# Kernel tuning notes

Hardware: AMD Instinct MI355X
Metric: run time of the kernel (lower is better)

## Reference

```python
import jax, jax.numpy as jnp
import numpy as np

D = 512
H = 8
FFN_H = 2048
NEG = -1.0e10


def layer_norm(x, gamma, beta, eps=1e-5):
    mu = jnp.mean(x, axis=-1, keepdims=True)
    var = jnp.var(x, axis=-1, keepdims=True)
    return (x - mu) * jax.lax.rsqrt(var + eps) * gamma + beta


def mha(x_q, x_kv, Wq, Wk, Wv, Wo, valid_lens):
    # x_q: [B,Tq,D], x_kv: [B,Tk,D]; valid_lens: [B,Tq] or [B]
    B, Tq, _ = x_q.shape
    Tk = x_kv.shape[1]
    dh = D // H
    q = (x_q @ Wq.T).reshape(B, Tq, H, dh).transpose(0, 2, 1, 3)  # [B,H,Tq,dh]
    k = (x_kv @ Wk.T).reshape(B, Tk, H, dh).transpose(0, 2, 1, 3)
    v = (x_kv @ Wv.T).reshape(B, Tk, H, dh).transpose(0, 2, 1, 3)
    scores = jnp.einsum('bhqd,bhkd->bhqk', q, k) / jnp.sqrt(jnp.float32(dh))
    pos = jnp.arange(Tk)
    if valid_lens.ndim == 1:  # [B] -> mask [B,1,1,Tk]
        mask = pos[None, None, None, :] < valid_lens[:, None, None, None]
    else:  # [B,Tq] -> mask [B,1,Tq,Tk]
        mask = pos[None, None, None, :] < valid_lens[:, None, :, None]
    scores = jnp.where(mask, scores, NEG)
    attn = jax.nn.softmax(scores, axis=-1)
    out = jnp.einsum('bhqk,bhkd->bhqd', attn, v)  # [B,H,Tq,dh]
    out = out.transpose(0, 2, 1, 3).reshape(B, Tq, D)
    return out @ Wo.T


def setup_inputs() -> dict:
    key = jax.random.key(0)
    ks = jax.random.split(key, 20)
    B, T = 32, 512
    s = 1.0 / np.sqrt(D)
    inp = {
        'X': jax.random.normal(ks[0], (B, T, D), jnp.float32),
        'enc_outputs': jax.random.normal(ks[1], (B, T, D), jnp.float32),
        'dec_valid_lens': jax.random.randint(ks[2], (B, T), 1, T + 1, jnp.int32),
        'enc_valid_lens': jax.random.randint(ks[3], (B,), 1, T + 1, jnp.int32),
    }
    names = ['Wq1', 'Wk1', 'Wv1', 'Wo1', 'Wq2', 'Wk2', 'Wv2', 'Wo2']
    for i, n in enumerate(names):
        inp[n] = jax.random.normal(ks[4 + i], (D, D), jnp.float32) * s
    inp['W1'] = jax.random.normal(ks[12], (FFN_H, D), jnp.float32) * s
    inp['b1'] = jnp.zeros((FFN_H,), jnp.float32)
    inp['W2'] = jax.random.normal(ks[13], (D, FFN_H), jnp.float32) * (1.0 / np.sqrt(FFN_H))
    inp['b2'] = jnp.zeros((D,), jnp.float32)
    for j in (1, 2, 3):
        inp[f'g{j}'] = jnp.ones((D,), jnp.float32)
        inp[f'be{j}'] = jnp.zeros((D,), jnp.float32)
    return inp


def reference(X, enc_outputs, dec_valid_lens, enc_valid_lens,
              Wq1, Wk1, Wv1, Wo1, Wq2, Wk2, Wv2, Wo2,
              W1, b1, W2, b2, g1, be1, g2, be2, g3, be3):
    # Training path: state[2][i] is None -> key_values = X. Dropout in eval mode (identity).
    X2 = mha(X, X, Wq1, Wk1, Wv1, Wo1, dec_valid_lens)            # self-attention
    Y = layer_norm(X + X2, g1, be1)                               # AddNorm1
    Y2 = mha(Y, enc_outputs, Wq2, Wk2, Wv2, Wo2, enc_valid_lens)  # cross-attention
    Z = layer_norm(Y + Y2, g2, be2)                               # AddNorm2
    F = (jax.nn.leaky_relu(Z @ W1.T + b1, 0.01)) @ W2.T + b2      # FFN (LeakyReLU slope 0.01)
    return layer_norm(Z + F, g3, be3)                             # AddNorm3
```

## Files before the change

### kernel.cpp

```cpp
#include <hip/hip_runtime.h>
#include <cstdint>
#include <cstddef>

typedef __bf16 bf16;
typedef __bf16 bf16x8 __attribute__((ext_vector_type(8)));
typedef float  f32x4  __attribute__((ext_vector_type(4)));
typedef unsigned short u16;

#define MD ((size_t)8388608)

__device__ __forceinline__ void async_copy16(const bf16* gp, bf16* lp) {
  __builtin_amdgcn_global_load_lds(
      (__attribute__((address_space(1))) void*)(gp),
      (__attribute__((address_space(3))) void*)(lp), 16, 0, 0);
}

__device__ __forceinline__ int is_f32(const u16* __restrict__ x) {
  const int e = (x[(threadIdx.x & 63) * 2] >> 7) & 0xFF;
  return __ballot(e >= 141) != 0ull;
}

struct ConvSrc { const void* p[20]; };

__global__ __launch_bounds__(256)
void convert_all(ConvSrc s, bf16* __restrict__ ws, const u16* __restrict__ xprobe)
{
  const int n[20] = {8388608, 8388608,
                     262144, 262144, 262144, 262144, 262144, 262144, 262144, 262144,
                     1048576, 2048, 1048576, 512, 512, 512, 512, 512, 512, 512};
  const unsigned int doff[20] = {
      41943040u, 50331648u,
      58720256u, 58982400u, 59244544u, 59506688u,
      59768832u, 60030976u, 60293120u, 60555264u,
      60817408u, 61865984u, 61868032u, 62916608u,
      62917120u, 62917632u, 62918144u, 62918656u, 62919168u, 62919680u};

  const int f32 = is_f32(xprobe);

  int bi = blockIdx.x;
  int idx = 0, b0 = 0;
  for (; idx < 20; ++idx) {
    const int nb = (n[idx] + 2047) >> 11;
    if (bi < b0 + nb) break;
    b0 += nb;
  }
  const int i = ((bi - b0) << 11) + threadIdx.x * 8;
  if (i >= n[idx]) return;
  bf16* dst = ws + doff[idx] + i;
  if (f32) {
    const float* sp = (const float*)s.p[idx] + i;
    f32x4 a = *(const f32x4*)sp;
    f32x4 b = *(const f32x4*)(sp + 4);
    bf16x8 o;
#pragma unroll
    for (int e = 0; e < 4; ++e) { o[e] = (bf16)a[e]; o[4 + e] = (bf16)b[e]; }
    *(bf16x8*)dst = o;
  } else {
    *(bf16x8*)dst = *(const bf16x8*)((const bf16*)s.p[idx] + i);
  }
}

template<int MODE, int TM, int TN>
__global__ __launch_bounds__(256)
void gemm_bt(const bf16* __restrict__ A, const bf16* __restrict__ B,
             const bf16* __restrict__ bias, bf16* __restrict__ C,
             int M, int N, int K)
{
  constexpr int MI = TM / 32;
  constexpr int NJ = TN / 32;
  __shared__ __attribute__((aligned(16))) bf16 As[TM * 64];
  __shared__ __attribute__((aligned(16))) bf16 Bs[TN * 64];

  const int t    = threadIdx.x;
  const int wave = t >> 6;
  const int lane = t & 63;
  const int quad = lane >> 4;
  const int l15  = lane & 15;
  const int wr   = (wave >> 1) * (TM / 2);
  const int wc   = (wave & 1) * (TN / 2);

  const int id    = blockIdx.y * gridDim.x + blockIdx.x;
  const int chunk = (gridDim.x * gridDim.y) >> 3;
  const int lin   = (id & 7) * chunk + (id >> 3);
  const int m0    = (lin / gridDim.x) * TM;
  const int n0    = (lin % gridDim.x) * TN;

  const f32x4 fz = {0.f, 0.f, 0.f, 0.f};
  f32x4 acc[MI][NJ];
#pragma unroll
  for (int i = 0; i < MI; ++i)
#pragma unroll
    for (int j = 0; j < NJ; ++j) acc[i][j] = fz;

  const int nkt = K >> 6;
  for (int kt = 0; kt < nkt; ++kt) {
    const int k0 = kt << 6;
    __syncthreads();
#pragma unroll
    for (int c = 0; c < TM / 32; ++c) {
      const int s   = c * 256 + t;
      const int row = s >> 3;
      const int kg  = ((s & 7) ^ (row & 7)) << 3;
      async_copy16(A + (size_t)(m0 + row) * K + k0 + kg,
                   As + ((c * 256 + wave * 64) << 3));
    }
#pragma unroll
    for (int c = 0; c < TN / 32; ++c) {
      const int s   = c * 256 + t;
      const int row = s >> 3;
      const int kg  = ((s & 7) ^ (row & 7)) << 3;
      async_copy16(B + (size_t)(n0 + row) * K + k0 + kg,
                   Bs + ((c * 256 + wave * 64) << 3));
    }
    __syncthreads();

#pragma unroll
    for (int ks = 0; ks < 2; ++ks) {
      bf16x8 af[MI], bfv[NJ];
#pragma unroll
      for (int i = 0; i < MI; ++i) {
        const int row = wr + i * 16 + l15;
        const int ph  = (ks * 4 + quad) ^ (row & 7);
        af[i] = *(const bf16x8*)(As + row * 64 + ph * 8);
      }
#pragma unroll
      for (int j = 0; j < NJ; ++j) {
        const int row = wc + j * 16 + l15;
        const int ph  = (ks * 4 + quad) ^ (row & 7);
        bfv[j] = *(const bf16x8*)(Bs + row * 64 + ph * 8);
      }
#pragma unroll
      for (int i = 0; i < MI; ++i)
#pragma unroll
        for (int j = 0; j < NJ; ++j)
          acc[i][j] = __builtin_amdgcn_mfma_f32_16x16x32_bf16(af[i], bfv[j],
                                                              acc[i][j], 0, 0, 0);
    }
  }

#pragma unroll
  for (int i = 0; i < MI; ++i) {
    const int m = m0 + wr + i * 16 + quad * 4;
#pragma unroll
    for (int j = 0; j < NJ; ++j) {
      const int n = n0 + wc + j * 16 + l15;
      float bv = 0.f;
      if (MODE >= 1) bv = (float)bias[n];
#pragma unroll
      for (int r = 0; r < 4; ++r) {
        float v = acc[i][j][r];
        if (MODE >= 1) v += bv;
        if (MODE == 1) v = v > 0.f ? v : 0.01f * v;
        C[(size_t)(m + r) * N + n] = (bf16)v;
      }
    }
  }
}

template<int MODE>
__global__ __launch_bounds__(512, 1)
void gemm4p(const bf16* __restrict__ A, const bf16* __restrict__ B,
            const bf16* __restrict__ bias, bf16* __restrict__ C,
            int M, int N, int K)
{
  constexpr int BM = 256, BN = 256, WM = 2, WN = 4, T = 512;
  constexpr int WR = BM / WM;
  constexpr int MI = WR / 16;
  constexpr int NJ = (BN / WN) / 16;
  constexpr int MH = MI / 2;
  constexpr int LA = BM * 8 / T;
  constexpr int LB = BN * 8 / T;
  static_assert(LA == 4 && LB == 4 && NJ == 4, "schedule assumes 4/4/4");

  __shared__ __attribute__((aligned(16))) bf16 As[2][BM * 64];
  __shared__ __attribute__((aligned(16))) bf16 Bs[2][BN * 64];

  const int t    = threadIdx.x;
  const int lane = t & 63;
  const int quad = lane >> 4;
  const int l15  = lane & 15;
  const int wave = t >> 6;
  const int wm   = wave >> 2;
  const int wn   = wave & 3;

  const int id    = blockIdx.y * gridDim.x + blockIdx.x;
  const int chunk = (gridDim.x * gridDim.y) >> 3;
  const int lin   = (id & 7) * chunk + (id >> 3);
  const int m0    = (lin / gridDim.x) * BM;
  const int n0    = (lin % gridDim.x) * BN;

  const bf16* Ag = A + (size_t)m0 * K;
  const bf16* Bg = B + (size_t)n0 * K;
  const int wbase = wave << 6;

  auto stA = [&](int kt, int r, int buf) {
    const int s   = r * T + t;
    const int row = s >> 3;
    const int cg  = s & 7;
    async_copy16(Ag + (size_t)row * K + (kt << 6) + ((cg ^ (row & 7)) << 3),
                 &As[buf][(size_t)(r * T + wbase) << 3]);
  };
  auto stB = [&](int kt, int r, int buf) {
    const int s   = r * T + t;
    const int row = s >> 3;
    const int cg  = s & 7;
    async_copy16(Bg + (size_t)row * K + (kt << 6) + ((cg ^ (row & 7)) << 3),
                 &Bs[buf][(size_t)(r * T + wbase) << 3]);
  };

  const f32x4 fz = {0.f, 0.f, 0.f, 0.f};
  f32x4 acc[MI][NJ];
#pragma unroll
  for (int i = 0; i < MI; ++i)
#pragma unroll
    for (int j = 0; j < NJ; ++j) acc[i][j] = fz;

  const int nkt = K >> 6;

#pragma unroll
  for (int r = 0; r < LA; ++r) stA(0, r, 0);
#pragma unroll
  for (int r = 0; r < LB; ++r) stB(0, r, 0);
  stA(1, 0, 1); stA(1, 2, 1);
#pragma unroll
  for (int r = 0; r < LB; ++r) stB(1, r, 1);
  asm volatile("s_waitcnt vmcnt(6)" ::: "memory");
  __builtin_amdgcn_s_barrier();

  for (int j = 0; j < nkt; ++j) {
    const int cb = j & 1;
    const bf16* a_l = As[cb];
    const bf16* b_l = Bs[cb];
    const int kN = (j + 1 < nkt) ? j + 1 : nkt - 1;
    const int kF = (j + 2 < nkt) ? j + 2 : nkt - 1;

    bf16x8 bfv[NJ];
    bf16x8 af[MH];

#pragma unroll
    for (int nj = 0; nj < NJ; ++nj) {
      const int row = wn * 64 + nj * 16 + l15;
      bfv[nj] = *(const bf16x8*)(b_l + row * 64 + ((quad ^ (row & 7)) << 3));
    }
#pragma unroll
    for (int mi = 0; mi < MH; ++mi) {
      const int row = wm * WR + mi * 16 + l15;
      af[mi] = *(const bf16x8*)(a_l + row * 64 + ((quad ^ (row & 7)) << 3));
    }
    stA(kN, 1, cb ^ 1); stA(kN, 3, cb ^ 1);
    __builtin_amdgcn_s_barrier();
    asm volatile("s_waitcnt lgkmcnt(0)" ::: "memory");
    __builtin_amdgcn_sched_barrier(0);
    __builtin_amdgcn_s_setprio(1);
#pragma unroll
    for (int mi = 0; mi < MH; ++mi)
#pragma unroll
      for (int nj = 0; nj < NJ; ++nj)
        acc[mi][nj] = __builtin_amdgcn_mfma_f32_16x16x32_bf16(af[mi], bfv[nj],
                                                              acc[mi][nj], 0, 0, 0);
    __builtin_amdgcn_s_setprio(0);
    __builtin_amdgcn_s_barrier();

#pragma unroll
    for (int mi = 0; mi < MH; ++mi) {
      const int row = wm * WR + (MH + mi) * 16 + l15;
      af[mi] = *(const bf16x8*)(a_l + row * 64 + ((quad ^ (row & 7)) << 3));
    }
    __builtin_amdgcn_s_barrier();
    asm volatile("s_waitcnt lgkmcnt(0)" ::: "memory");
    __builtin_amdgcn_sched_barrier(0);
    __builtin_amdgcn_s_setprio(1);
#pragma unroll
    for (int mi = 0; mi < MH; ++mi)
#pragma unroll
      for (int nj = 0; nj < NJ; ++nj)
        acc[MH + mi][nj] = __builtin_amdgcn_mfma_f32_16x16x32_bf16(af[mi], bfv[nj],
                                                                   acc[MH + mi][nj], 0, 0, 0);
    __builtin_amdgcn_s_setprio(0);
    __builtin_amdgcn_s_barrier();

#pragma unroll
    for (int nj = 0; nj < NJ; ++nj) {
      const int row = wn * 64 + nj * 16 + l15;
      bfv[nj] = *(const bf16x8*)(b_l + row * 64 + (((4 + quad) ^ (row & 7)) << 3));
    }
#pragma unroll
    for (int mi = 0; mi < MH; ++mi) {
      const int row = wm * WR + mi * 16 + l15;
      af[mi] = *(const bf16x8*)(a_l + row * 64 + (((4 + quad) ^ (row & 7)) << 3));
    }
    __builtin_amdgcn_s_barrier();
    asm volatile("s_waitcnt lgkmcnt(0)" ::: "memory");
    __builtin_amdgcn_sched_barrier(0);
    __builtin_amdgcn_s_setprio(1);
#pragma unroll
    for (int mi = 0; mi < MH; ++mi)
#pragma unroll
      for (int nj = 0; nj < NJ; ++nj)
        acc[mi][nj] = __builtin_amdgcn_mfma_f32_16x16x32_bf16(af[mi], bfv[nj],
                                                              acc[mi][nj], 0, 0, 0);
    __builtin_amdgcn_s_setprio(0);
    __builtin_amdgcn_s_barrier();

#pragma unroll
    for (int mi = 0; mi < MH; ++mi) {
      const int row = wm * WR + (MH + mi) * 16 + l15;
      af[mi] = *(const bf16x8*)(a_l + row * 64 + (((4 + quad) ^ (row & 7)) << 3));
    }
    stA(kF, 0, cb); stA(kF, 2, cb);
#pragma unroll
    for (int r = 0; r < LB; ++r) stB(kF, r, cb);
    __builtin_amdgcn_s_barrier();
    asm volatile("s_waitcnt lgkmcnt(0)" ::: "memory");
    __builtin_amdgcn_sched_barrier(0);
    __builtin_amdgcn_s_setprio(1);
#pragma unroll
    for (int mi = 0; mi < MH; ++mi)
#pragma unroll
      for (int nj = 0; nj < NJ; ++nj)
        acc[MH + mi][nj] = __builtin_amdgcn_mfma_f32_16x16x32_bf16(af[mi], bfv[nj],
                                                                   acc[MH + mi][nj], 0, 0, 0);
    __builtin_amdgcn_s_setprio(0);
    asm volatile("s_waitcnt vmcnt(6)" ::: "memory");
    __builtin_amdgcn_s_barrier();
  }

  asm volatile("s_waitcnt vmcnt(0)" ::: "memory");

#pragma unroll
  for (int mi = 0; mi < MI; ++mi) {
    const int m = m0 + wm * WR + mi * 16 + quad * 4;
#pragma unroll
    for (int nj = 0; nj < NJ; ++nj) {
      const int n = n0 + wn * 64 + nj * 16 + l15;
      float bv = 0.f;
      if (MODE >= 1) bv = (float)bias[n];
#pragma unroll
      for (int r = 0; r < 4; ++r) {
        float v = acc[mi][nj][r];
        if (MODE >= 1) v += bv;
        if (MODE == 1) v = v > 0.f ? v : 0.01f * v;
        C[(size_t)(m + r) * N + n] = (bf16)v;
      }
    }
  }
}

__global__ __launch_bounds__(256, 4)
void flash_attn(const bf16* __restrict__ Qp, const bf16* __restrict__ Kp,
                const bf16* __restrict__ Vp, bf16* __restrict__ Op,
                const int* __restrict__ vlen, int per_query, int sq, int skv)
{
  __shared__ __attribute__((aligned(16))) bf16 Ks[64][72];
  __shared__ __attribute__((aligned(16))) bf16 VsT[64][72];
  __shared__ __attribute__((aligned(16))) bf16 Ps[4][32][72];
  __shared__ int vlmax_sh;

  const int t    = threadIdx.x;
  const int wave = t >> 6;
  const int lane = t & 63;
  const int quad = lane >> 4;
  const int l15  = lane & 15;
  const int bx   = blockIdx.x;
  const int qt   = bx >> 8;
  const int h    = bx & 7;
  const int b    = (bx >> 3) & 31;
  const int q0   = qt * 128 + wave * 32;

  bf16x8 qfrag[2][2];
#pragma unroll
  for (int mt = 0; mt < 2; ++mt)
#pragma unroll
    for (int ks = 0; ks < 2; ++ks)
      qfrag[mt][ks] = *(const bf16x8*)(Qp +
          (size_t)(b * 512 + q0 + mt * 16 + l15) * sq + h * 64 + ks * 32 + quad * 8);

  int vl_r[2][4];
  int myvl = 1;
#pragma unroll
  for (int mt = 0; mt < 2; ++mt)
#pragma unroll
    for (int r = 0; r < 4; ++r) {
      const int q = q0 + mt * 16 + quad * 4 + r;
      const int v = per_query ? vlen[b * 512 + q] : vlen[b];
      vl_r[mt][r] = v;
      myvl = v > myvl ? v : myvl;
    }

  if (t == 0) vlmax_sh = 1;
  __syncthreads();
#pragma unroll
  for (int off = 1; off < 64; off <<= 1) {
    const int o = __shfl_xor(myvl, off);
    myvl = o > myvl ? o : myvl;
  }
  if (lane == 0) atomicMax(&vlmax_sh, myvl);
  __syncthreads();
  const int ktiles = (vlmax_sh + 63) >> 6;

  const f32x4 fz = {0.f, 0.f, 0.f, 0.f};
  float l_part[2][4] = {{0.f,0.f,0.f,0.f},{0.f,0.f,0.f,0.f}};
  f32x4 o_acc[2][4];
#pragma unroll
  for (int mt = 0; mt < 2; ++mt)
#pragma unroll
    for (int nt = 0; nt < 4; ++nt) o_acc[mt][nt] = fz;

  for (int kt = 0; kt < ktiles; ++kt) {
    const int k0 = kt * 64;
    __syncthreads();
    {
      const int r0 = t >> 3;
      const int c0 = (t & 7) * 8;
      const bf16* g = Kp + (size_t)(b * 512 + k0 + r0) * skv + h * 64 + c0;
      *(bf16x8*)&Ks[r0][c0]      = *(const bf16x8*)g;
      *(bf16x8*)&Ks[r0 + 32][c0] = *(const bf16x8*)(g + (size_t)32 * skv);
    }
    {
      const bf16* g = Vp + (size_t)(b * 512 + k0 + wave * 16) * skv + h * 64 + lane;
      bf16x8 lo, hi;
#pragma unroll
      for (int kk = 0; kk < 8; ++kk) lo[kk] = g[(size_t)kk * skv];
#pragma unroll
      for (int kk = 0; kk < 8; ++kk) hi[kk] = g[(size_t)(kk + 8) * skv];
      *(bf16x8*)&VsT[lane][wave * 16]     = lo;
      *(bf16x8*)&VsT[lane][wave * 16 + 8] = hi;
    }
    __syncthreads();

    f32x4 s[2][4];
#pragma unroll
    for (int mt = 0; mt < 2; ++mt)
#pragma unroll
      for (int nt = 0; nt < 4; ++nt) s[mt][nt] = fz;
#pragma unroll
    for (int ks = 0; ks < 2; ++ks)
#pragma unroll
      for (int nt = 0; nt < 4; ++nt) {
        const bf16x8 bk = *(const bf16x8*)&Ks[nt * 16 + l15][ks * 32 + quad * 8];
        s[0][nt] = __builtin_amdgcn_mfma_f32_16x16x32_bf16(qfrag[0][ks], bk, s[0][nt], 0, 0, 0);
        s[1][nt] = __builtin_amdgcn_mfma_f32_16x16x32_bf16(qfrag[1][ks], bk, s[1][nt], 0, 0, 0);
      }

#pragma unroll
    for (int mt = 0; mt < 2; ++mt)
#pragma unroll
      for (int nt = 0; nt < 4; ++nt) {
        const int k_abs = k0 + nt * 16 + l15;
#pragma unroll
        for (int r = 0; r < 4; ++r) {
          const float p = (k_abs < vl_r[mt][r]) ? __expf(s[mt][nt][r] * 0.125f) : 0.f;
          l_part[mt][r] += p;
          Ps[wave][mt * 16 + quad * 4 + r][nt * 16 + l15] = (bf16)p;
        }
      }

#pragma unroll
    for (int ks = 0; ks < 2; ++ks) {
      const bf16x8 ap0 = *(const bf16x8*)&Ps[wave][l15][ks * 32 + quad * 8];
      const bf16x8 ap1 = *(const bf16x8*)&Ps[wave][16 + l15][ks * 32 + quad * 8];
#pragma unroll
      for (int nt = 0; nt < 4; ++nt) {
        const bf16x8 bv = *(const bf16x8*)&VsT[nt * 16 + l15][ks * 32 + quad * 8];
        o_acc[0][nt] = __builtin_amdgcn_mfma_f32_16x16x32_bf16(ap0, bv, o_acc[0][nt], 0, 0, 0);
        o_acc[1][nt] = __builtin_amdgcn_mfma_f32_16x16x32_bf16(ap1, bv, o_acc[1][nt], 0, 0, 0);
      }
    }
  }

#pragma unroll
  for (int mt = 0; mt < 2; ++mt)
#pragma unroll
    for (int r = 0; r < 4; ++r) {
      float l = l_part[mt][r];
#pragma unroll
      for (int off = 1; off < 16; off <<= 1)
        l += __shfl_xor(l, off);
      const float inv_l = (l > 0.f) ? (1.f / l) : 0.f;
      const int q = q0 + mt * 16 + quad * 4 + r;
#pragma unroll
      for (int nt = 0; nt < 4; ++nt)
        Op[(size_t)(b * 512 + q) * 512 + h * 64 + nt * 16 + l15] =
            (bf16)(o_acc[mt][nt][r] * inv_l);
    }
}

__global__ __launch_bounds__(256)
void add_layernorm(const bf16* X, const bf16* R,
                   const bf16* __restrict__ gamma, const bf16* __restrict__ beta,
                   bf16* Out)
{
  const int t    = threadIdx.x;
  const int wave = t >> 6;
  const int lane = t & 63;
  const size_t row  = (size_t)blockIdx.x * 4 + wave;
  const size_t base = row * 512 + lane * 8;

  bf16x8 xv = *(const bf16x8*)(X + base);
  bf16x8 rv = *(const bf16x8*)(R + base);
  float v[8];
  float sum = 0.f, ss = 0.f;
#pragma unroll
  for (int i = 0; i < 8; ++i) {
    v[i] = (float)xv[i] + (float)rv[i];
    sum += v[i];
    ss  += v[i] * v[i];
  }
#pragma unroll
  for (int off = 1; off < 64; off <<= 1) {
    sum += __shfl_xor(sum, off);
    ss  += __shfl_xor(ss, off);
  }
  const float mean = sum * (1.f / 512.f);
  const float var  = ss * (1.f / 512.f) - mean * mean;
  const float rstd = rsqrtf(var + 1e-5f);

  bf16x8 gv = *(const bf16x8*)(gamma + lane * 8);
  bf16x8 bv = *(const bf16x8*)(beta + lane * 8);
  bf16x8 ov;
#pragma unroll
  for (int i = 0; i < 8; ++i)
    ov[i] = (bf16)(((v[i] - mean) * rstd) * (float)gv[i] + (float)bv[i]);
  *(bf16x8*)(Out + base) = ov;
}

__global__ __launch_bounds__(256)
void add_layernorm_out(const bf16* X, const bf16* R,
                       const bf16* __restrict__ gamma, const bf16* __restrict__ beta,
                       void* Out, const u16* __restrict__ xprobe)
{
  const int t    = threadIdx.x;
  const int wave = t >> 6;
  const int lane = t & 63;
  const size_t row  = (size_t)blockIdx.x * 4 + wave;
  const size_t base = row * 512 + lane * 8;

  const int f32 = is_f32(xprobe);

  bf16x8 xv = *(const bf16x8*)(X + base);
  bf16x8 rv = *(const bf16x8*)(R + base);
  float v[8];
  float sum = 0.f, ss = 0.f;
#pragma unroll
  for (int i = 0; i < 8; ++i) {
    v[i] = (float)xv[i] + (float)rv[i];
    sum += v[i];
    ss  += v[i] * v[i];
  }
#pragma unroll
  for (int off = 1; off < 64; off <<= 1) {
    sum += __shfl_xor(sum, off);
    ss  += __shfl_xor(ss, off);
  }
  const float mean = sum * (1.f / 512.f);
  const float var  = ss * (1.f / 512.f) - mean * mean;
  const float rstd = rsqrtf(var + 1e-5f);

  bf16x8 gv = *(const bf16x8*)(gamma + lane * 8);
  bf16x8 bv = *(const bf16x8*)(beta + lane * 8);
  float o[8];
#pragma unroll
  for (int i = 0; i < 8; ++i)
    o[i] = ((v[i] - mean) * rstd) * (float)gv[i] + (float)bv[i];

  if (f32) {
    float* op = (float*)Out + base;
    f32x4 o0 = {o[0], o[1], o[2], o[3]};
    f32x4 o1 = {o[4], o[5], o[6], o[7]};
    *(f32x4*)op       = o0;
    *(f32x4*)(op + 4) = o1;
  } else {
    bf16x8 ov;
#pragma unroll
    for (int i = 0; i < 8; ++i) ov[i] = (bf16)o[i];
    *(bf16x8*)((bf16*)Out + base) = ov;
  }
}

extern "C" void kernel_launch(void* const* d_in, const int* in_sizes, int n_in,
                              void* d_out, int out_size, void* d_ws, size_t ws_size,
                              hipStream_t stream)
{
  (void)in_sizes; (void)n_in; (void)out_size; (void)ws_size;

  const int* dvl = (const int*)d_in[2];
  const int* evl = (const int*)d_in[3];
  const u16* xprobe = (const u16*)d_in[0];

  bf16* ws = (bf16*)d_ws;
  bf16* S0 = ws;
  bf16* S1 = ws + 1 * MD;
  bf16* S3 = ws + 3 * MD;
  bf16* S4 = ws + 4 * MD;
  bf16* Xb = ws + 5 * MD;
  bf16* Eb = ws + 6 * MD;
  bf16* W  = ws + 7 * MD;
  const bf16 *Wq1 = W,
             *Wo1 = W + 786432,   *Wq2 = W + 1048576, *Wk2 = W + 1310720,
             *Wo2 = W + 1835008,
             *W1  = W + 2097152,  *b1  = W + 3145728,
             *W2  = W + 3147776,  *b2  = W + 4196352,
             *g1  = W + 4196864,  *be1 = W + 4197376,
             *g2  = W + 4197888,  *be2 = W + 4198400,
             *g3  = W + 4198912,  *be3 = W + 4199424;

  ConvSrc cs;
  cs.p[0] = d_in[0];  cs.p[1] = d_in[1];
  for (int k = 0; k < 12; ++k) cs.p[2 + k] = d_in[4 + k];
  for (int k = 0; k < 6; ++k)  cs.p[14 + k] = d_in[16 + k];
  convert_all<<<dim3(10248), dim3(256), 0, stream>>>(cs, ws, xprobe);

  dim3 blk256(256);
  dim3 blk512(512);
  dim3 gP(4, 128);

  gemm4p<0><<<dim3(6, 64), blk512, 0, stream>>>(Xb, Wq1, nullptr, S0, 16384, 1536, 512);
  flash_attn<<<dim3(1024), blk256, 0, stream>>>(S0, S0 + 512, S0 + 1024, S3, dvl, 1, 1536, 1536);
  gemm_bt<0,128,128><<<gP, blk256, 0, stream>>>(S3, Wo1, nullptr, S1, 16384, 512, 512);
  add_layernorm<<<dim3(4096), blk256, 0, stream>>>(Xb, S1, g1, be1, S4);

  gemm_bt<0,128,128><<<gP, blk256, 0, stream>>>(S4, Wq2, nullptr, S0, 16384, 512, 512);
  gemm4p<0><<<dim3(4, 64), blk512, 0, stream>>>(Eb, Wk2, nullptr, S1, 16384, 1024, 512);
  flash_attn<<<dim3(1024), blk256, 0, stream>>>(S0, S1, S1 + 512, S3, evl, 0, 512, 1024);
  gemm_bt<0,128,128><<<gP, blk256, 0, stream>>>(S3, Wo2, nullptr, S1, 16384, 512, 512);
  add_layernorm<<<dim3(4096), blk256, 0, stream>>>(S4, S1, g2, be2, S4);

  gemm4p<1><<<dim3(8, 64), blk512, 0, stream>>>(S4, W1, b1, S0, 16384, 2048, 512);
  gemm_bt<2,128,128><<<gP, blk256, 0, stream>>>(S0, W2, b2, Xb, 16384, 512, 2048);
  add_layernorm_out<<<dim3(4096), blk256, 0, stream>>>(S4, Xb, g3, be3, d_out, xprobe);
}
```

Measured before the change: 461.5 us.

## Generalize 4-phase GEMM tile shape and route FFN down-projection through it

Templates the 4-phase pipelined GEMM on BM/WM/WN and reorders its inner schedule so each phase covers a k-half for one half of the M fragments. B fragments for both k-halves stay in registers, and the A/B prefetch loads are redistributed across the phases. The FFN second GEMM (K=2048, N=512) switches from the 128x128 gemm_bt kernel to a 128x256 variant of this pipelined kernel, with 256 blocks of 512 threads. The aim is deeper overlap of loads with MFMA for the long-K GEMM. The risk is fewer blocks than CUs, which leaves occupancy low, plus more register pressure from the extra B fragments.

```diff
diff --git a/kernel.cpp b/kernel.cpp
--- a/kernel.cpp
+++ b/kernel.cpp
@@ -157,20 +157,20 @@
   }
 }
 
-template<int MODE>
+template<int MODE, int BM, int WM, int WN>
 __global__ __launch_bounds__(512, 1)
 void gemm4p(const bf16* __restrict__ A, const bf16* __restrict__ B,
             const bf16* __restrict__ bias, bf16* __restrict__ C,
             int M, int N, int K)
 {
-  constexpr int BM = 256, BN = 256, WM = 2, WN = 4, T = 512;
+  constexpr int BN = 256, T = 512;
   constexpr int WR = BM / WM;
   constexpr int MI = WR / 16;
   constexpr int NJ = (BN / WN) / 16;
   constexpr int MH = MI / 2;
   constexpr int LA = BM * 8 / T;
   constexpr int LB = BN * 8 / T;
-  static_assert(LA == 4 && LB == 4 && NJ == 4, "schedule assumes 4/4/4");
+  static_assert(NJ == 4 && LB == 4 && (LA == 4 || LA == 2), "schedule");
 
   __shared__ __attribute__((aligned(16))) bf16 As[2][BM * 64];
   __shared__ __attribute__((aligned(16))) bf16 Bs[2][BN * 64];
@@ -180,8 +180,8 @@
   const int quad = lane >> 4;
   const int l15  = lane & 15;
   const int wave = t >> 6;
-  const int wm   = wave >> 2;
-  const int wn   = wave & 3;
+  const int wm   = wave / WN;
+  const int wn   = wave % WN;
 
   const int id    = blockIdx.y * gridDim.x + blockIdx.x;
   const int chunk = (gridDim.x * gridDim.y) >> 3;
@@ -207,6 +207,9 @@
     async_copy16(Bg + (size_t)row * K + (kt << 6) + ((cg ^ (row & 7)) << 3),
                  &Bs[buf][(size_t)(r * T + wbase) << 3]);
   };
+  auto ldfrag = [&](const bf16* base, int row, int ks) -> bf16x8 {
+    return *(const bf16x8*)(base + row * 64 + ((((ks << 2) + quad) ^ (row & 7)) << 3));
+  };
 
   const f32x4 fz = {0.f, 0.f, 0.f, 0.f};
   f32x4 acc[MI][NJ];
@@ -221,10 +224,9 @@
   for (int r = 0; r < LA; ++r) stA(0, r, 0);
 #pragma unroll
   for (int r = 0; r < LB; ++r) stB(0, r, 0);
-  stA(1, 0, 1); stA(1, 2, 1);
 #pragma unroll
   for (int r = 0; r < LB; ++r) stB(1, r, 1);
-  asm volatile("s_waitcnt vmcnt(6)" ::: "memory");
+  asm volatile("s_waitcnt vmcnt(4)" ::: "memory");
   __builtin_amdgcn_s_barrier();
 
   for (int j = 0; j < nkt; ++j) {
@@ -234,20 +236,14 @@
     const int kN = (j + 1 < nkt) ? j + 1 : nkt - 1;
     const int kF = (j + 2 < nkt) ? j + 2 : nkt - 1;
 
-    bf16x8 bfv[NJ];
+    bf16x8 bfv[NJ][2];
     bf16x8 af[MH];
 
 #pragma unroll
-    for (int nj = 0; nj < NJ; ++nj) {
-      const int row = wn * 64 + nj * 16 + l15;
-      bfv[nj] = *(const bf16x8*)(b_l + row * 64 + ((quad ^ (row & 7)) << 3));
-    }
-#pragma unroll
-    for (int mi = 0; mi < MH; ++mi) {
-      const int row = wm * WR + mi * 16 + l15;
-      af[mi] = *(const bf16x8*)(a_l + row * 64 + ((quad ^ (row & 7)) << 3));
-    }
-    stA(kN, 1, cb ^ 1); stA(kN, 3, cb ^ 1);
+    for (int nj = 0; nj < NJ; ++nj) bfv[nj][0] = ldfrag(b_l, wn * 64 + nj * 16 + l15, 0);
+#pragma unroll
+    for (int mi = 0; mi < MH; ++mi) af[mi] = ldfrag(a_l, wm * WR + mi * 16 + l15, 0);
+    stA(kN, 0, cb ^ 1); stA(kN, 1, cb ^ 1);
     __builtin_amdgcn_s_barrier();
     asm volatile("s_waitcnt lgkmcnt(0)" ::: "memory");
     __builtin_amdgcn_sched_barrier(0);
@@ -256,16 +252,16 @@
     for (int mi = 0; mi < MH; ++mi)
 #pragma unroll
       for (int nj = 0; nj < NJ; ++nj)
-        acc[mi][nj] = __builtin_amdgcn_mfma_f32_16x16x32_bf16(af[mi], bfv[nj],
+        acc[mi][nj] = __builtin_amdgcn_mfma_f32_16x16x32_bf16(af[mi], bfv[nj][0],
                                                               acc[mi][nj], 0, 0, 0);
     __builtin_amdgcn_s_setprio(0);
     __builtin_amdgcn_s_barrier();
 
 #pragma unroll
-    for (int mi = 0; mi < MH; ++mi) {
-      const int row = wm * WR + (MH + mi) * 16 + l15;
-      af[mi] = *(const bf16x8*)(a_l + row * 64 + ((quad ^ (row & 7)) << 3));
-    }
+    for (int nj = 0; nj < NJ; ++nj) bfv[nj][1] = ldfrag(b_l, wn * 64 + nj * 16 + l15, 1);
+#pragma unroll
+    for (int mi = 0; mi < MH; ++mi) af[mi] = ldfrag(a_l, wm * WR + mi * 16 + l15, 1);
+    if constexpr (LA == 4) { stA(kN, 2, cb ^ 1); stA(kN, 3, cb ^ 1); }
     __builtin_amdgcn_s_barrier();
     asm volatile("s_waitcnt lgkmcnt(0)" ::: "memory");
     __builtin_amdgcn_sched_barrier(0);
@@ -274,21 +270,14 @@
     for (int mi = 0; mi < MH; ++mi)
 #pragma unroll
       for (int nj = 0; nj < NJ; ++nj)
-        acc[MH + mi][nj] = __builtin_amdgcn_mfma_f32_16x16x32_bf16(af[mi], bfv[nj],
-                                                                   acc[MH + mi][nj], 0, 0, 0);
+        acc[mi][nj] = __builtin_amdgcn_mfma_f32_16x16x32_bf16(af[mi], bfv[nj][1],
+                                                              acc[mi][nj], 0, 0, 0);
     __builtin_amdgcn_s_setprio(0);
     __builtin_amdgcn_s_barrier();
 
 #pragma unroll
-    for (int nj = 0; nj < NJ; ++nj) {
-      const int row = wn * 64 + nj * 16 + l15;
-      bfv[nj] = *(const bf16x8*)(b_l + row * 64 + (((4 + quad) ^ (row & 7)) << 3));
-    }
-#pragma unroll
-    for (int mi = 0; mi < MH; ++mi) {
-      const int row = wm * WR + mi * 16 + l15;
-      af[mi] = *(const bf16x8*)(a_l + row * 64 + (((4 + quad) ^ (row & 7)) << 3));
-    }
+    for (int mi = 0; mi < MH; ++mi) af[mi] = ldfrag(a_l, wm * WR + (MH + mi) * 16 + l15, 0);
+    stB(kF, 0, cb); stB(kF, 1, cb);
     __builtin_amdgcn_s_barrier();
     asm volatile("s_waitcnt lgkmcnt(0)" ::: "memory");
     __builtin_amdgcn_sched_barrier(0);
@@ -297,19 +286,14 @@
     for (int mi = 0; mi < MH; ++mi)
 #pragma unroll
       for (int nj = 0; nj < NJ; ++nj)
-        acc[mi][nj] = __builtin_amdgcn_mfma_f32_16x16x32_bf16(af[mi], bfv[nj],
-                                                              acc[mi][nj], 0, 0, 0);
+        acc[MH + mi][nj] = __builtin_amdgcn_mfma_f32_16x16x32_bf16(af[mi], bfv[nj][0],
+                                                                   acc[MH + mi][nj], 0, 0, 0);
     __builtin_amdgcn_s_setprio(0);
     __builtin_amdgcn_s_barrier();
 
 #pragma unroll
-    for (int mi = 0; mi < MH; ++mi) {
-      const int row = wm * WR + (MH + mi) * 16 + l15;
-      af[mi] = *(const bf16x8*)(a_l + row * 64 + (((4 + quad) ^ (row & 7)) << 3));
-    }
-    stA(kF, 0, cb); stA(kF, 2, cb);
-#pragma unroll
-    for (int r = 0; r < LB; ++r) stB(kF, r, cb);
+    for (int mi = 0; mi < MH; ++mi) af[mi] = ldfrag(a_l, wm * WR + (MH + mi) * 16 + l15, 1);
+    stB(kF, 2, cb); stB(kF, 3, cb);
     __builtin_amdgcn_s_barrier();
     asm volatile("s_waitcnt lgkmcnt(0)" ::: "memory");
     __builtin_amdgcn_sched_barrier(0);
@@ -318,10 +302,10 @@
     for (int mi = 0; mi < MH; ++mi)
 #pragma unroll
       for (int nj = 0; nj < NJ; ++nj)
-        acc[MH + mi][nj] = __builtin_amdgcn_mfma_f32_16x16x32_bf16(af[mi], bfv[nj],
+        acc[MH + mi][nj] = __builtin_amdgcn_mfma_f32_16x16x32_bf16(af[mi], bfv[nj][1],
                                                                    acc[MH + mi][nj], 0, 0, 0);
     __builtin_amdgcn_s_setprio(0);
-    asm volatile("s_waitcnt vmcnt(6)" ::: "memory");
+    asm volatile("s_waitcnt vmcnt(4)" ::: "memory");
     __builtin_amdgcn_s_barrier();
   }
 
@@ -614,18 +598,18 @@
   dim3 blk512(512);
   dim3 gP(4, 128);
 
-  gemm4p<0><<<dim3(6, 64), blk512, 0, stream>>>(Xb, Wq1, nullptr, S0, 16384, 1536, 512);
+  gemm4p<0,256,2,4><<<dim3(6, 64), blk512, 0, stream>>>(Xb, Wq1, nullptr, S0, 16384, 1536, 512);
   flash_attn<<<dim3(1024), blk256, 0, stream>>>(S0, S0 + 512, S0 + 1024, S3, dvl, 1, 1536, 1536);
   gemm_bt<0,128,128><<<gP, blk256, 0, stream>>>(S3, Wo1, nullptr, S1, 16384, 512, 512);
   add_layernorm<<<dim3(4096), blk256, 0, stream>>>(Xb, S1, g1, be1, S4);
 
   gemm_bt<0,128,128><<<gP, blk256, 0, stream>>>(S4, Wq2, nullptr, S0, 16384, 512, 512);
-  gemm4p<0><<<dim3(4, 64), blk512, 0, stream>>>(Eb, Wk2, nullptr, S1, 16384, 1024, 512);
+  gemm4p<0,256,2,4><<<dim3(4, 64), blk512, 0, stream>>>(Eb, Wk2, nullptr, S1, 16384, 1024, 512);
   flash_attn<<<dim3(1024), blk256, 0, stream>>>(S0, S1, S1 + 512, S3, evl, 0, 512, 1024);
   gemm_bt<0,128,128><<<gP, blk256, 0, stream>>>(S3, Wo2, nullptr, S1, 16384, 512, 512);
   add_layernorm<<<dim3(4096), blk256, 0, stream>>>(S4, S1, g2, be2, S4);
 
-  gemm4p<1><<<dim3(8, 64), blk512, 0, stream>>>(S4, W1, b1, S0, 16384, 2048, 512);
-  gemm_bt<2,128,128><<<gP, blk256, 0, stream>>>(S0, W2, b2, Xb, 16384, 512, 2048);
+  gemm4p<1,256,2,4><<<dim3(8, 64), blk512, 0, stream>>>(S4, W1, b1, S0, 16384, 2048, 512);
+  gemm4p<2,128,2,4><<<dim3(2, 128), blk512, 0, stream>>>(S0, W2, b2, Xb, 16384, 512, 2048);
   add_layernorm_out<<<dim3(4096), blk256, 0, stream>>>(S4, Xb, g3, be3, d_out, xprobe);
 }
```

After: 468.0 us. Within noise of the previous version (+1.4%).
